# Optimization experiments

Measured on AMD Instinct MI355X. Metric: run time of the kernel, lower is better.

The kernel has to match this reference:

```python
import jax, jax.numpy as jnp
import numpy as np

MSK_TOK_ID = 4
SPC_TOK_IDS = (0, 1, 2, 3)
REG_W, MSK_W, SPC_W = 1.0, 1.0, 0.01
B, S, V = 8, 1024, 32000


def setup_inputs() -> dict:
    key = jax.random.key(0)
    k1, k2, k3 = jax.random.split(key, 3)
    logits_pred = jax.random.normal(k1, (B, S, V), dtype=jnp.float32)
    tokens_inp = jax.random.randint(k2, (B, S), 0, 100, dtype=jnp.int32)
    tokens_tgt = jax.random.randint(k3, (B, S), 0, V, dtype=jnp.int32)
    return {"logits_pred": logits_pred, "tokens_inp": tokens_inp, "tokens_tgt": tokens_tgt}


def _loss(logits_pred, tokens_inp, tokens_tgt):
    # torch: softmax then log(gather) == log_softmax then gather (more stable, same math)
    logp = jax.nn.log_softmax(logits_pred, axis=-1)                 # [B,S,V]
    nll = -jnp.take_along_axis(logp, tokens_tgt[..., None].astype(jnp.int32), axis=2)[..., 0]  # [B,S]

    mask_msk = tokens_inp == MSK_TOK_ID
    mask_spc = jnp.zeros_like(mask_msk)
    for t in SPC_TOK_IDS:
        mask_spc = mask_spc | (tokens_inp == t)
    mask_reg = (~mask_msk) & (~mask_spc)

    def cat_mean(mask):
        cnt = jnp.sum(mask, axis=1)                                  # [B]
        s = jnp.sum(jnp.where(mask, nll, 0.0), axis=1)               # [B]
        present = cnt > 0
        mean = jnp.where(present, s / jnp.maximum(cnt, 1).astype(nll.dtype), 0.0)
        return mean, present.astype(nll.dtype)

    m_reg, p_reg = cat_mean(mask_reg)
    m_msk, p_msk = cat_mean(mask_msk)
    m_spc, p_spc = cat_mean(mask_spc)

    num = m_reg * REG_W * p_reg + m_msk * MSK_W * p_msk + m_spc * SPC_W * p_spc
    tw = p_reg * REG_W + p_msk * MSK_W + p_spc * SPC_W              # per-item total_weight
    loss = jnp.mean(num / tw)

    def cat_avg(mean, present):
        n = jnp.sum(present)
        return jnp.where(n > 0, jnp.sum(mean) / jnp.maximum(n, 1.0), 0.0)

    return loss, cat_avg(m_reg, p_reg), cat_avg(m_msk, p_msk), cat_avg(m_spc, p_spc)


def reference(logits_pred, tokens_inp, tokens_tgt):
    # returns (loss, reg_toks_loss, msk_toks_loss, spc_toks_loss)
    return _loss(logits_pred, tokens_inp, tokens_tgt)
```

## Files before the change

kernel.cpp:

```cpp
#include <hip/hip_runtime.h>
#include <math.h>

#define NB 8
#define NS 1024
#define NV 32000

__global__ __launch_bounds__(256)
void nll_kernel(const float* __restrict__ logits,
                const int* __restrict__ tgt,
                float* __restrict__ nll) {
    const int row = blockIdx.x;
    const float* rp = logits + (size_t)row * NV;
    const int tid = threadIdx.x;
    const float4* rp4 = (const float4*)rp;
    const int n4 = NV / 4;

    float s0 = 0.f, s1 = 0.f;
    for (int i = tid; i < n4; i += 256) {
        float4 x = rp4[i];
        float e0 = __expf(x.x);
        float e1 = __expf(x.y);
        float e2 = __expf(x.z);
        float e3 = __expf(x.w);
        s0 += e0 + e1;
        s1 += e2 + e3;
    }
    float s = s0 + s1;

    #pragma unroll
    for (int off = 1; off < 64; off <<= 1)
        s += __shfl_xor(s, off, 64);

    __shared__ float ssum[4];
    __shared__ float blk_s;
    const int wave = tid >> 6, lane = tid & 63;
    if (lane == 0) ssum[wave] = s;
    __syncthreads();
    if (tid == 0) blk_s = (ssum[0] + ssum[1]) + (ssum[2] + ssum[3]);
    __syncthreads();
    const float S = blk_s;

    if (S > 1.0e-30f && S < 3.0e38f) {
        if (tid == 0) nll[row] = __logf(S) - rp[tgt[row]];
        return;
    }

    float m = -INFINITY;
    for (int i = tid; i < n4; i += 256) {
        float4 x = rp4[i];
        m = fmaxf(m, fmaxf(fmaxf(x.x, x.y), fmaxf(x.z, x.w)));
    }
    #pragma unroll
    for (int off = 1; off < 64; off <<= 1)
        m = fmaxf(m, __shfl_xor(m, off, 64));
    __shared__ float smax[4];
    __shared__ float blk_m;
    if (lane == 0) smax[wave] = m;
    __syncthreads();
    if (tid == 0)
        blk_m = fmaxf(fmaxf(smax[0], smax[1]), fmaxf(smax[2], smax[3]));
    __syncthreads();
    const float M = blk_m;

    float c0 = 0.f, c1 = 0.f;
    for (int i = tid; i < n4; i += 256) {
        float4 x = rp4[i];
        c0 += __expf(x.x - M) + __expf(x.y - M);
        c1 += __expf(x.z - M) + __expf(x.w - M);
    }
    float c = c0 + c1;
    #pragma unroll
    for (int off = 1; off < 64; off <<= 1)
        c += __shfl_xor(c, off, 64);
    if (lane == 0) ssum[wave] = c;
    __syncthreads();
    if (tid == 0) {
        float S2 = (ssum[0] + ssum[1]) + (ssum[2] + ssum[3]);
        nll[row] = M + __logf(S2) - rp[tgt[row]];
    }
}

__global__ __launch_bounds__(512)
void reduce_finalize_kernel(const int* __restrict__ inp,
                            const float* __restrict__ nll,
                            float* __restrict__ out) {
    const int tid = threadIdx.x;
    const int b = tid >> 6;
    const int lane = tid & 63;
    const int base = b * NS;

    float acc[6] = {0.f, 0.f, 0.f, 0.f, 0.f, 0.f};
    for (int i = lane; i < NS; i += 64) {
        int tok = inp[base + i];
        float v = nll[base + i];
        if (tok == 4)                { acc[2] += v; acc[3] += 1.f; }
        else if ((unsigned)tok < 4u) { acc[4] += v; acc[5] += 1.f; }
        else                         { acc[0] += v; acc[1] += 1.f; }
    }
    #pragma unroll
    for (int off = 1; off < 64; off <<= 1) {
        #pragma unroll
        for (int k = 0; k < 6; ++k) acc[k] += __shfl_xor(acc[k], off, 64);
    }

    __shared__ float part[NB][6];
    if (lane == 0) {
        #pragma unroll
        for (int k = 0; k < 6; ++k) part[b][k] = acc[k];
    }
    __syncthreads();

    if (tid == 0) {
        const float W[3] = {1.0f, 1.0f, 0.01f};
        float loss_acc = 0.f;
        float sum_m[3] = {0.f, 0.f, 0.f};
        float sum_p[3] = {0.f, 0.f, 0.f};
        for (int bb = 0; bb < NB; ++bb) {
            float num = 0.f, tw = 0.f;
            #pragma unroll
            for (int k = 0; k < 3; ++k) {
                float sv = part[bb][2 * k];
                float cn = part[bb][2 * k + 1];
                float p = (cn > 0.f) ? 1.f : 0.f;
                float mean = (cn > 0.f) ? (sv / cn) : 0.f;
                num += mean * W[k] * p;
                tw  += p * W[k];
                sum_m[k] += mean;
                sum_p[k] += p;
            }
            loss_acc += num / tw;
        }
        out[0] = loss_acc / (float)NB;
        #pragma unroll
        for (int k = 0; k < 3; ++k)
            out[1 + k] = (sum_p[k] > 0.f) ? (sum_m[k] / fmaxf(sum_p[k], 1.f))
                                          : 0.f;
    }
}

extern "C" void kernel_launch(void* const* d_in, const int* in_sizes, int n_in,
                              void* d_out, int out_size, void* d_ws, size_t ws_size,
                              hipStream_t stream) {
    const float* logits = (const float*)d_in[0];
    const int*   inp    = (const int*)d_in[1];
    const int*   tgt    = (const int*)d_in[2];
    float* out = (float*)d_out;
    float* nll = (float*)d_ws;

    nll_kernel<<<NB * NS, 256, 0, stream>>>(logits, tgt, nll);
    reduce_finalize_kernel<<<1, 512, 0, stream>>>(inp, nll, out);
}
```

Measured before the change: 194.1 us.

## Fuse NLL and reduction into one kernel with wave-per-row and atomic finalize

Each wave now handles one full row, so the block-level shared-memory reductions and barriers are removed and a block covers four rows. Per-batch, per-category NLL sums are accumulated with 64-bit fixed-point atomics, and the last block to finish, detected through an atomic counter, computes the final outputs. This drops the second kernel launch and the workspace round trip for the per-row NLL values. In exchange it adds a memset, atomic contention on 24 counters, and rounding error from the 2^24 fixed-point scale.

```diff
diff --git a/kernel.cpp b/kernel.cpp
--- a/kernel.cpp
+++ b/kernel.cpp
@@ -4,137 +4,112 @@
 #define NB 8
 #define NS 1024
 #define NV 32000
+#define NROWS (NB * NS)
+#define RPB 4
+#define NBLK (NROWS / RPB)
+#define N4 (NV / 4)
+#define ITERS (N4 / 64)
+#define FXSCALE 16777216.0f
+
 
 __global__ __launch_bounds__(256)
-void nll_kernel(const float* __restrict__ logits,
-                const int* __restrict__ tgt,
-                float* __restrict__ nll) {
-    const int row = blockIdx.x;
+void fused_loss_kernel(const float* __restrict__ logits,
+                       const int* __restrict__ inp,
+                       const int* __restrict__ tgt,
+                       float* __restrict__ out,
+                       unsigned long long* __restrict__ sums,
+                       unsigned int* __restrict__ cnts,
+                       unsigned int* __restrict__ ctr) {
+    const int wave = threadIdx.x >> 6;
+    const int lane = threadIdx.x & 63;
+    const int row = blockIdx.x * RPB + wave;
     const float* rp = logits + (size_t)row * NV;
-    const int tid = threadIdx.x;
     const float4* rp4 = (const float4*)rp;
-    const int n4 = NV / 4;
+
+    const float lt = rp[tgt[row]];
 
     float s0 = 0.f, s1 = 0.f;
-    for (int i = tid; i < n4; i += 256) {
+    int i = lane;
+    #pragma unroll 5
+    for (int it = 0; it < ITERS; ++it, i += 64) {
         float4 x = rp4[i];
-        float e0 = __expf(x.x);
-        float e1 = __expf(x.y);
-        float e2 = __expf(x.z);
-        float e3 = __expf(x.w);
-        s0 += e0 + e1;
-        s1 += e2 + e3;
+        s0 += __expf(x.x) + __expf(x.y);
+        s1 += __expf(x.z) + __expf(x.w);
     }
     float s = s0 + s1;
-
     #pragma unroll
     for (int off = 1; off < 64; off <<= 1)
         s += __shfl_xor(s, off, 64);
 
-    __shared__ float ssum[4];
-    __shared__ float blk_s;
-    const int wave = tid >> 6, lane = tid & 63;
-    if (lane == 0) ssum[wave] = s;
-    __syncthreads();
-    if (tid == 0) blk_s = (ssum[0] + ssum[1]) + (ssum[2] + ssum[3]);
-    __syncthreads();
-    const float S = blk_s;
-
-    if (S > 1.0e-30f && S < 3.0e38f) {
-        if (tid == 0) nll[row] = __logf(S) - rp[tgt[row]];
-        return;
+    float nllv;
+    if (s > 1.0e-30f && s < 3.0e38f) {
+        nllv = __logf(s) - lt;
+    } else {
+        float m = -INFINITY;
+        int j = lane;
+        for (int it = 0; it < ITERS; ++it, j += 64) {
+            float4 x = rp4[j];
+            m = fmaxf(m, fmaxf(fmaxf(x.x, x.y), fmaxf(x.z, x.w)));
+        }
+        #pragma unroll
+        for (int off = 1; off < 64; off <<= 1)
+            m = fmaxf(m, __shfl_xor(m, off, 64));
+        float c0 = 0.f, c1 = 0.f;
+        j = lane;
+        for (int it = 0; it < ITERS; ++it, j += 64) {
+            float4 x = rp4[j];
+            c0 += __expf(x.x - m) + __expf(x.y - m);
+            c1 += __expf(x.z - m) + __expf(x.w - m);
+        }
+        float c = c0 + c1;
+        #pragma unroll
+        for (int off = 1; off < 64; off <<= 1)
+            c += __shfl_xor(c, off, 64);
+        nllv = m + __logf(c) - lt;
     }
 
-    float m = -INFINITY;
-    for (int i = tid; i < n4; i += 256) {
-        float4 x = rp4[i];
-        m = fmaxf(m, fmaxf(fmaxf(x.x, x.y), fmaxf(x.z, x.w)));
-    }
-    #pragma unroll
-    for (int off = 1; off < 64; off <<= 1)
-        m = fmaxf(m, __shfl_xor(m, off, 64));
-    __shared__ float smax[4];
-    __shared__ float blk_m;
-    if (lane == 0) smax[wave] = m;
-    __syncthreads();
-    if (tid == 0)
-        blk_m = fmaxf(fmaxf(smax[0], smax[1]), fmaxf(smax[2], smax[3]));
-    __syncthreads();
-    const float M = blk_m;
-
-    float c0 = 0.f, c1 = 0.f;
-    for (int i = tid; i < n4; i += 256) {
-        float4 x = rp4[i];
-        c0 += __expf(x.x - M) + __expf(x.y - M);
-        c1 += __expf(x.z - M) + __expf(x.w - M);
-    }
-    float c = c0 + c1;
-    #pragma unroll
-    for (int off = 1; off < 64; off <<= 1)
-        c += __shfl_xor(c, off, 64);
-    if (lane == 0) ssum[wave] = c;
-    __syncthreads();
-    if (tid == 0) {
-        float S2 = (ssum[0] + ssum[1]) + (ssum[2] + ssum[3]);
-        nll[row] = M + __logf(S2) - rp[tgt[row]];
-    }
-}
-
-__global__ __launch_bounds__(512)
-void reduce_finalize_kernel(const int* __restrict__ inp,
-                            const float* __restrict__ nll,
-                            float* __restrict__ out) {
-    const int tid = threadIdx.x;
-    const int b = tid >> 6;
-    const int lane = tid & 63;
-    const int base = b * NS;
-
-    float acc[6] = {0.f, 0.f, 0.f, 0.f, 0.f, 0.f};
-    for (int i = lane; i < NS; i += 64) {
-        int tok = inp[base + i];
-        float v = nll[base + i];
-        if (tok == 4)                { acc[2] += v; acc[3] += 1.f; }
-        else if ((unsigned)tok < 4u) { acc[4] += v; acc[5] += 1.f; }
-        else                         { acc[0] += v; acc[1] += 1.f; }
-    }
-    #pragma unroll
-    for (int off = 1; off < 64; off <<= 1) {
-        #pragma unroll
-        for (int k = 0; k < 6; ++k) acc[k] += __shfl_xor(acc[k], off, 64);
+    if (lane == 0) {
+        int tok = inp[row];
+        int k = (tok == 4) ? 1 : (((unsigned)tok < 4u) ? 2 : 0);
+        int b = row >> 10;
+        long long q = (long long)(nllv * FXSCALE);
+        atomicAdd(&sums[b * 3 + k], (unsigned long long)q);
+        atomicAdd(&cnts[b * 3 + k], 1u);
     }
 
-    __shared__ float part[NB][6];
-    if (lane == 0) {
-        #pragma unroll
-        for (int k = 0; k < 6; ++k) part[b][k] = acc[k];
-    }
     __syncthreads();
-
-    if (tid == 0) {
-        const float W[3] = {1.0f, 1.0f, 0.01f};
-        float loss_acc = 0.f;
-        float sum_m[3] = {0.f, 0.f, 0.f};
-        float sum_p[3] = {0.f, 0.f, 0.f};
-        for (int bb = 0; bb < NB; ++bb) {
-            float num = 0.f, tw = 0.f;
+    if (threadIdx.x == 0) {
+        __threadfence();
+        unsigned int old = atomicAdd(ctr, 1u);
+        if (old == (unsigned int)(gridDim.x - 1)) {
+            const float W[3] = {1.0f, 1.0f, 0.01f};
+            float loss_acc = 0.f;
+            float sum_m[3] = {0.f, 0.f, 0.f};
+            float sum_p[3] = {0.f, 0.f, 0.f};
+            for (int bb = 0; bb < NB; ++bb) {
+                float num = 0.f, tw = 0.f;
+                #pragma unroll
+                for (int k = 0; k < 3; ++k) {
+                    long long sll =
+                        (long long)atomicAdd(&sums[bb * 3 + k], 0ull);
+                    unsigned int cn = atomicAdd(&cnts[bb * 3 + k], 0u);
+                    float sv = (float)((double)sll / 16777216.0);
+                    float p = (cn > 0u) ? 1.f : 0.f;
+                    float mean = (cn > 0u) ? (sv / (float)cn) : 0.f;
+                    num += mean * W[k] * p;
+                    tw  += p * W[k];
+                    sum_m[k] += mean;
+                    sum_p[k] += p;
+                }
+                loss_acc += num / tw;
+            }
+            out[0] = loss_acc / (float)NB;
             #pragma unroll
-            for (int k = 0; k < 3; ++k) {
-                float sv = part[bb][2 * k];
-                float cn = part[bb][2 * k + 1];
-                float p = (cn > 0.f) ? 1.f : 0.f;
-                float mean = (cn > 0.f) ? (sv / cn) : 0.f;
-                num += mean * W[k] * p;
-                tw  += p * W[k];
-                sum_m[k] += mean;
-                sum_p[k] += p;
-            }
-            loss_acc += num / tw;
+            for (int k = 0; k < 3; ++k)
+                out[1 + k] = (sum_p[k] > 0.f)
+                                 ? (sum_m[k] / fmaxf(sum_p[k], 1.f))
+                                 : 0.f;
         }
-        out[0] = loss_acc / (float)NB;
-        #pragma unroll
-        for (int k = 0; k < 3; ++k)
-            out[1 + k] = (sum_p[k] > 0.f) ? (sum_m[k] / fmaxf(sum_p[k], 1.f))
-                                          : 0.f;
     }
 }
 
@@ -145,8 +120,12 @@
     const int*   inp    = (const int*)d_in[1];
     const int*   tgt    = (const int*)d_in[2];
     float* out = (float*)d_out;
-    float* nll = (float*)d_ws;
 
-    nll_kernel<<<NB * NS, 256, 0, stream>>>(logits, tgt, nll);
-    reduce_finalize_kernel<<<1, 512, 0, stream>>>(inp, nll, out);
+    unsigned long long* sums = (unsigned long long*)d_ws;
+    unsigned int* cnts = (unsigned int*)(sums + NB * 3);
+    unsigned int* ctr  = cnts + NB * 3;
+
+    hipMemsetAsync(d_ws, 0, 512, stream);
+    fused_loss_kernel<<<NBLK, 256, 0, stream>>>(logits, inp, tgt,
+                                                out, sums, cnts, ctr);
 }
```

Result: slower. 284.3 us (+46.5%).
